# Performance work log

Hardware: AMD Instinct MI355X
Metric: run time of the kernel (lower is better)

## Reference

```python
import jax, jax.numpy as jnp
import numpy as np

B, T, D = 4096, 8, 2048
EPS = 1e-5


def setup_inputs() -> dict:
    key = jax.random.key(0)
    ks = jax.random.split(key, 7)
    s = 1.0 / np.sqrt(D)  # xavier-ish scale
    return {
        "H": jax.random.normal(ks[0], (B, T, D), jnp.float32),
        "Wq": jax.random.normal(ks[1], (T, D, D), jnp.float32) * s,
        "Wk": jax.random.normal(ks[2], (D, D), jnp.float32) * s,
        "Wv": jax.random.normal(ks[3], (D, D), jnp.float32) * s,
        "Wg": jax.random.normal(ks[4], (T, D, D), jnp.float32) * s,
        "bg": jnp.zeros((T, D), jnp.float32),
        "gamma": jnp.ones((T, D), jnp.float32),
        "beta": jnp.zeros((T, D), jnp.float32),
    }


def reference(H, Wq, Wk, Wv, Wg, bg, gamma, beta):
    # H: (B, T, D) = stacked task_reprs. Linear uses y = x @ W.T.
    scale = jnp.sqrt(jnp.asarray(D, H.dtype))
    K = jnp.einsum('bsd,ed->bse', H, Wk)          # (B, T, D) shared keys
    V = jnp.einsum('bsd,ed->bse', H, Wv)          # (B, T, D) shared values
    Q = jnp.einsum('btd,ted->bte', H, Wq)         # per-task query projection
    scores = jnp.einsum('bte,bse->bts', Q, K) / scale  # (B, T, T)
    attn = jax.nn.softmax(scores, axis=-1)
    ctx = jnp.einsum('bts,bse->bte', attn, V)     # (B, T, D)
    # dropout is identity at eval time
    g = jax.nn.sigmoid(jnp.einsum('btd,ted->bte', H, Wg) + bg)  # per-task gate
    x = H + g * ctx                               # gated residual
    mu = jnp.mean(x, axis=-1, keepdims=True)
    var = jnp.var(x, axis=-1, keepdims=True)
    out = (x - mu) / jnp.sqrt(var + EPS) * gamma + beta  # per-task LayerNorm
    return out
```

## Files before the change

kernel.cpp:

```cpp
#include <hip/hip_runtime.h>
#include <cstdint>

typedef unsigned short u16;
typedef uint32_t u32;
typedef float f32x4 __attribute__((ext_vector_type(4)));
typedef __bf16 bf16x8 __attribute__((ext_vector_type(8)));

#define GLDS16(gp, lp)                                                                   \
  __builtin_amdgcn_global_load_lds((const __attribute__((address_space(1))) void*)(gp),  \
                                   (__attribute__((address_space(3))) void*)(lp), 16, 0, 0)

__device__ __forceinline__ float blo(u32 u) { return __uint_as_float(u << 16); }
__device__ __forceinline__ float bhi(u32 u) { return __uint_as_float(u & 0xFFFF0000u); }
__device__ __forceinline__ u16 f2b(float f) {
  u32 u = __float_as_uint(f);
  u32 r = u + 0x7FFFu + ((u >> 16) & 1u);
  return (u16)(r >> 16);
}

__global__ __launch_bounds__(256) void ctil_cvt_f2b(
    const float* __restrict__ in, u16* __restrict__ out, long n)
{
  long i = ((long)blockIdx.x * blockDim.x + threadIdx.x) * 8;
  const long stride = (long)gridDim.x * blockDim.x * 8;
  for (; i < n; i += stride) {
    float4 a = *reinterpret_cast<const float4*>(in + i);
    float4 b = *reinterpret_cast<const float4*>(in + i + 4);
    uint4 o;
    o.x = (u32)f2b(a.x) | ((u32)f2b(a.y) << 16);
    o.y = (u32)f2b(a.z) | ((u32)f2b(a.w) << 16);
    o.z = (u32)f2b(b.x) | ((u32)f2b(b.y) << 16);
    o.w = (u32)f2b(b.z) | ((u32)f2b(b.w) << 16);
    *reinterpret_cast<uint4*>(out + i) = o;
  }
}

__global__ __launch_bounds__(256) void ctil_gemm_bt(
    const u16* __restrict__ Hb, const u16* __restrict__ Wqb,
    const u16* __restrict__ Wkb, const u16* __restrict__ Wvb,
    const u16* __restrict__ Wgb,
    u16* __restrict__ Kb, u16* __restrict__ Vb,
    u16* __restrict__ Qb, u16* __restrict__ Gb,
    int zbase)
{
  const int z = blockIdx.z + zbase;
  const u16* A;
  const u16* W;
  u16* C;
  int lda, ldc;
  if (z < 2) {
    A = Hb; lda = 2048; ldc = 2048;
    W = (z == 0) ? Wkb : Wvb;
    C = (z == 0) ? Kb : Vb;
  } else {
    const int t = (z - 2) & 7;
    A = Hb + t * 2048; lda = 16384; ldc = 16384;
    W = ((z < 10) ? Wqb : Wgb) + (size_t)t * (size_t)(2048 * 2048);
    C = ((z < 10) ? Qb : Gb) + t * 2048;
  }
  const int bm = blockIdx.x, bn = blockIdx.y;
  const int tid = (int)threadIdx.x;
  const int lane = tid & 63, wid = tid >> 6;
  const int wm = wid >> 1, wn = wid & 1;

  __shared__ __align__(16) u16 As[128 * 32];
  __shared__ __align__(16) u16 Bs[128 * 32];

  const int srow = tid >> 2;
  const int scol = (tid & 3) * 8;
  const u16* Ag = A + (size_t)(bm * 128 + srow) * lda + scol;
  const u16* Bg = W + (size_t)(bn * 128 + srow) * 2048 + scol;
  u16* AsW = As + wid * 512;
  u16* BsW = Bs + wid * 512;

  f32x4 acc[4][4] = {};

  const int frow = lane & 15;
  const int fk = (lane >> 4) * 8;

  for (int kt = 0; kt < 2048; kt += 32) {
    GLDS16(Ag + kt, AsW);
    GLDS16(Ag + kt + (size_t)64 * lda, AsW + 2048);
    GLDS16(Bg + kt, BsW);
    GLDS16(Bg + kt + 64 * 2048, BsW + 2048);
    __syncthreads();

    bf16x8 af[4], bfr[4];
#pragma unroll
    for (int i = 0; i < 4; ++i)
      af[i] = *reinterpret_cast<const bf16x8*>(&As[(wm * 64 + i * 16 + frow) * 32 + fk]);
#pragma unroll
    for (int j = 0; j < 4; ++j)
      bfr[j] = *reinterpret_cast<const bf16x8*>(&Bs[(wn * 64 + j * 16 + frow) * 32 + fk]);
#pragma unroll
    for (int i = 0; i < 4; ++i)
#pragma unroll
      for (int j = 0; j < 4; ++j)
        acc[i][j] = __builtin_amdgcn_mfma_f32_16x16x32_bf16(af[i], bfr[j], acc[i][j], 0, 0, 0);
    __syncthreads();
  }

  const int cl = lane & 15, chq = lane >> 4;
#pragma unroll
  for (int i = 0; i < 4; ++i) {
#pragma unroll
    for (int r = 0; r < 4; ++r) {
      const int row = bm * 128 + wm * 64 + i * 16 + chq * 4 + r;
      u16* Cr = C + (size_t)row * ldc + bn * 128 + wn * 64 + cl;
#pragma unroll
      for (int j = 0; j < 4; ++j)
        Cr[j * 16] = f2b(acc[i][j][r]);
    }
  }
}

__global__ __launch_bounds__(256) void ctil_epilogue(
    const u16* __restrict__ Hb, const u16* __restrict__ Kb,
    const u16* __restrict__ Vb, const u16* __restrict__ Qb,
    const u16* __restrict__ Gb, const float* __restrict__ bgp,
    const float* __restrict__ gap, const float* __restrict__ bep,
    float* __restrict__ Out)
{
  const int b = blockIdx.x;
  const int tid = (int)threadIdx.x;
  const int lane = tid & 63, wid = tid >> 6;
  const size_t rbase = (size_t)b * 16384;
  const int e0 = tid * 8;

  __shared__ float red[256];
  __shared__ float r1s[4], r2s[4];

  u32 qw[8][4], kw[8][4];
#pragma unroll
  for (int t = 0; t < 8; ++t) {
    uint4 v = *reinterpret_cast<const uint4*>(Qb + rbase + t * 2048 + e0);
    qw[t][0] = v.x; qw[t][1] = v.y; qw[t][2] = v.z; qw[t][3] = v.w;
    uint4 w = *reinterpret_cast<const uint4*>(Kb + rbase + t * 2048 + e0);
    kw[t][0] = w.x; kw[t][1] = w.y; kw[t][2] = w.z; kw[t][3] = w.w;
  }

  float sc[64];
#pragma unroll
  for (int p = 0; p < 64; ++p) sc[p] = 0.f;

#pragma unroll
  for (int c = 0; c < 4; ++c) {
    float ql[8], qh[8], kl[8], kh[8];
#pragma unroll
    for (int t = 0; t < 8; ++t) {
      ql[t] = blo(qw[t][c]); qh[t] = bhi(qw[t][c]);
      kl[t] = blo(kw[t][c]); kh[t] = bhi(kw[t][c]);
    }
#pragma unroll
    for (int t = 0; t < 8; ++t)
#pragma unroll
      for (int s = 0; s < 8; ++s)
        sc[t * 8 + s] += ql[t] * kl[s] + qh[t] * kh[s];
  }

#pragma unroll
  for (int p = 0; p < 64; ++p) {
    float v = sc[p];
#pragma unroll
    for (int m = 1; m < 64; m <<= 1) v += __shfl_xor(v, m, 64);
    sc[p] = v;
  }
  if (lane == 0) {
#pragma unroll
    for (int p = 0; p < 64; ++p) red[wid * 64 + p] = sc[p];
  }
  __syncthreads();

  const float INVS = 0.022097086912079608f;
#pragma unroll
  for (int p = 0; p < 64; ++p)
    sc[p] = (red[p] + red[64 + p] + red[128 + p] + red[192 + p]) * INVS;

#pragma unroll
  for (int t = 0; t < 8; ++t) {
    float m = sc[t * 8];
#pragma unroll
    for (int s = 1; s < 8; ++s) m = fmaxf(m, sc[t * 8 + s]);
    float l = 0.f;
#pragma unroll
    for (int s = 0; s < 8; ++s) {
      float e = __expf(sc[t * 8 + s] - m);
      sc[t * 8 + s] = e;
      l += e;
    }
    float inv = 1.f / l;
#pragma unroll
    for (int s = 0; s < 8; ++s) sc[t * 8 + s] *= inv;
  }

  u32 vw[8][4];
#pragma unroll
  for (int s = 0; s < 8; ++s) {
    uint4 v = *reinterpret_cast<const uint4*>(Vb + rbase + s * 2048 + e0);
    vw[s][0] = v.x; vw[s][1] = v.y; vw[s][2] = v.z; vw[s][3] = v.w;
  }

  for (int t = 0; t < 8; ++t) {
    float cx[8];
#pragma unroll
    for (int j = 0; j < 8; ++j) cx[j] = 0.f;
#pragma unroll
    for (int s = 0; s < 8; ++s) {
      float a = sc[t * 8 + s];
#pragma unroll
      for (int c = 0; c < 4; ++c) {
        cx[2 * c]     += a * blo(vw[s][c]);
        cx[2 * c + 1] += a * bhi(vw[s][c]);
      }
    }
    uint4 gu = *reinterpret_cast<const uint4*>(Gb + rbase + t * 2048 + e0);
    uint4 hu = *reinterpret_cast<const uint4*>(Hb + rbase + t * 2048 + e0);
    u32 ga[4] = {gu.x, gu.y, gu.z, gu.w};
    u32 ha[4] = {hu.x, hu.y, hu.z, hu.w};
    float bgv[8];
    *reinterpret_cast<float4*>(&bgv[0]) = *reinterpret_cast<const float4*>(bgp + t * 2048 + e0);
    *reinterpret_cast<float4*>(&bgv[4]) = *reinterpret_cast<const float4*>(bgp + t * 2048 + e0 + 4);
    float x[8];
    float s1 = 0.f, s2 = 0.f;
#pragma unroll
    for (int c = 0; c < 4; ++c) {
      float gl = blo(ga[c]) + bgv[2 * c];
      float gh = bhi(ga[c]) + bgv[2 * c + 1];
      float sgl = 1.f / (1.f + __expf(-gl));
      float sgh = 1.f / (1.f + __expf(-gh));
      float xl = blo(ha[c]) + sgl * cx[2 * c];
      float xh = bhi(ha[c]) + sgh * cx[2 * c + 1];
      x[2 * c] = xl; x[2 * c + 1] = xh;
      s1 += xl + xh;
      s2 += xl * xl + xh * xh;
    }
#pragma unroll
    for (int m = 1; m < 64; m <<= 1) {
      s1 += __shfl_xor(s1, m, 64);
      s2 += __shfl_xor(s2, m, 64);
    }
    if (lane == 0) { r1s[wid] = s1; r2s[wid] = s2; }
    __syncthreads();
    const float invD = 1.f / 2048.f;
    float S1 = r1s[0] + r1s[1] + r1s[2] + r1s[3];
    float S2 = r2s[0] + r2s[1] + r2s[2] + r2s[3];
    float mu = S1 * invD;
    float var = S2 * invD - mu * mu;
    float rstd = rsqrtf(var + 1e-5f);
    float gmv[8], btv[8];
    *reinterpret_cast<float4*>(&gmv[0]) = *reinterpret_cast<const float4*>(gap + t * 2048 + e0);
    *reinterpret_cast<float4*>(&gmv[4]) = *reinterpret_cast<const float4*>(gap + t * 2048 + e0 + 4);
    *reinterpret_cast<float4*>(&btv[0]) = *reinterpret_cast<const float4*>(bep + t * 2048 + e0);
    *reinterpret_cast<float4*>(&btv[4]) = *reinterpret_cast<const float4*>(bep + t * 2048 + e0 + 4);
    float4 o1, o2;
    o1.x = (x[0] - mu) * rstd * gmv[0] + btv[0];
    o1.y = (x[1] - mu) * rstd * gmv[1] + btv[1];
    o1.z = (x[2] - mu) * rstd * gmv[2] + btv[2];
    o1.w = (x[3] - mu) * rstd * gmv[3] + btv[3];
    o2.x = (x[4] - mu) * rstd * gmv[4] + btv[4];
    o2.y = (x[5] - mu) * rstd * gmv[5] + btv[5];
    o2.z = (x[6] - mu) * rstd * gmv[6] + btv[6];
    o2.w = (x[7] - mu) * rstd * gmv[7] + btv[7];
    *reinterpret_cast<float4*>(Out + rbase + t * 2048 + e0) = o1;
    *reinterpret_cast<float4*>(Out + rbase + t * 2048 + e0 + 4) = o2;
    __syncthreads();
  }
}

extern "C" void kernel_launch(void* const* d_in, const int* in_sizes, int n_in,
                              void* d_out, int out_size, void* d_ws, size_t ws_size,
                              hipStream_t stream)
{
  const float* H  = (const float*)d_in[0];
  const float* Wq = (const float*)d_in[1];
  const float* Wk = (const float*)d_in[2];
  const float* Wv = (const float*)d_in[3];
  const float* Wg = (const float*)d_in[4];
  const float* bg = (const float*)d_in[5];
  const float* ga = (const float*)d_in[6];
  const float* be = (const float*)d_in[7];
  float* Out = (float*)d_out;

  const size_t NWQ = 33554432, NWK = 4194304;
  u16* Wqb = (u16*)d_ws;
  u16* Wgb = Wqb + NWQ;
  u16* Wkb = Wgb + NWQ;
  u16* Wvb = Wkb + NWK;
  u16* chunkbase = Wvb + NWK;

  const size_t fixed = 150994944ull;
  int nch = 1;
  while (nch < 32 && fixed + (size_t)(4096 / nch) * 163840ull > ws_size) nch <<= 1;
  const int CB = 4096 / nch;

  u16* Hb = chunkbase;
  u16* Kw = Hb + (size_t)CB * 16384;
  u16* Vw = Kw + (size_t)CB * 16384;
  u16* Gw = Vw + (size_t)CB * 16384;
  u16* Qw = Gw + (size_t)CB * 16384;

  ctil_cvt_f2b<<<2048, 256, 0, stream>>>(Wq, Wqb, (long)NWQ);
  ctil_cvt_f2b<<<2048, 256, 0, stream>>>(Wg, Wgb, (long)NWQ);
  ctil_cvt_f2b<<<512, 256, 0, stream>>>(Wk, Wkb, (long)NWK);
  ctil_cvt_f2b<<<512, 256, 0, stream>>>(Wv, Wvb, (long)NWK);

  for (int c = 0; c < nch; ++c) {
    const size_t off = (size_t)c * (size_t)CB * 16384;
    ctil_cvt_f2b<<<2048, 256, 0, stream>>>(H + off, Hb, (long)CB * 16384);
    ctil_gemm_bt<<<dim3(CB / 16, 16, 2), 256, 0, stream>>>(
        Hb, Wqb, Wkb, Wvb, Wgb, Kw, Vw, Qw, Gw, 0);
    ctil_gemm_bt<<<dim3(CB / 128, 16, 16), 256, 0, stream>>>(
        Hb, Wqb, Wkb, Wvb, Wgb, Kw, Vw, Qw, Gw, 2);
    ctil_epilogue<<<dim3(CB), 256, 0, stream>>>(
        Hb, Kw, Vw, Qw, Gw, bg, ga, be, Out + off);
  }
}
```

Measured before the change: 1.839 ms.

## Replace bf16 GEMM with double-buffered 256x256-tile, 8-wave pipelined MFMA kernel

Replaces the 128x128, single-buffered GEMM with a 256x256-tile kernel using 512 threads and a 64-wide K step. Shared-memory stages are double-buffered with an XOR swizzle against bank conflicts. Global-to-LDS loads for the next K step are interleaved with four MFMA quadrants under explicit waitcnt, barriers and s_setprio. The goal is more data reuse per byte loaded and latency hiding that the old two-barrier loop lacked. The cost is 128KB of LDS per block, which limits occupancy, and the chunk count is capped at 16 so the tile divides the chunk.

```diff
diff --git a/kernel.cpp b/kernel.cpp
--- a/kernel.cpp
+++ b/kernel.cpp
@@ -35,7 +35,7 @@
   }
 }
 
-__global__ __launch_bounds__(256) void ctil_gemm_bt(
+__global__ __launch_bounds__(512, 2) void ctil_gemm256(
     const u16* __restrict__ Hb, const u16* __restrict__ Wqb,
     const u16* __restrict__ Wkb, const u16* __restrict__ Wvb,
     const u16* __restrict__ Wgb,
@@ -61,57 +61,147 @@
   const int bm = blockIdx.x, bn = blockIdx.y;
   const int tid = (int)threadIdx.x;
   const int lane = tid & 63, wid = tid >> 6;
-  const int wm = wid >> 1, wn = wid & 1;
-
-  __shared__ __align__(16) u16 As[128 * 32];
-  __shared__ __align__(16) u16 Bs[128 * 32];
-
-  const int srow = tid >> 2;
-  const int scol = (tid & 3) * 8;
-  const u16* Ag = A + (size_t)(bm * 128 + srow) * lda + scol;
-  const u16* Bg = W + (size_t)(bn * 128 + srow) * 2048 + scol;
-  u16* AsW = As + wid * 512;
-  u16* BsW = Bs + wid * 512;
-
-  f32x4 acc[4][4] = {};
-
-  const int frow = lane & 15;
-  const int fk = (lane >> 4) * 8;
-
-  for (int kt = 0; kt < 2048; kt += 32) {
-    GLDS16(Ag + kt, AsW);
-    GLDS16(Ag + kt + (size_t)64 * lda, AsW + 2048);
-    GLDS16(Bg + kt, BsW);
-    GLDS16(Bg + kt + 64 * 2048, BsW + 2048);
-    __syncthreads();
-
-    bf16x8 af[4], bfr[4];
-#pragma unroll
-    for (int i = 0; i < 4; ++i)
-      af[i] = *reinterpret_cast<const bf16x8*>(&As[(wm * 64 + i * 16 + frow) * 32 + fk]);
-#pragma unroll
-    for (int j = 0; j < 4; ++j)
-      bfr[j] = *reinterpret_cast<const bf16x8*>(&Bs[(wn * 64 + j * 16 + frow) * 32 + fk]);
-#pragma unroll
-    for (int i = 0; i < 4; ++i)
-#pragma unroll
-      for (int j = 0; j < 4; ++j)
-        acc[i][j] = __builtin_amdgcn_mfma_f32_16x16x32_bf16(af[i], bfr[j], acc[i][j], 0, 0, 0);
-    __syncthreads();
-  }
-
-  const int cl = lane & 15, chq = lane >> 4;
-#pragma unroll
-  for (int i = 0; i < 4; ++i) {
+  const int wm = wid >> 2, wn = wid & 3;
+
+  __shared__ __align__(16) u16 As[2][16384];
+  __shared__ __align__(16) u16 Bs[2][16384];
+
+  const int srl = lane >> 3;
+  const int sq  = (lane & 7) ^ srl;
+  const u16* Ag = A + (size_t)(bm * 256 + wid * 8 + srl) * lda + sq * 8;
+  const u16* Bg = W + (size_t)(bn * 256 + wid * 8 + srl) * 2048 + sq * 8;
+
+#define STAGE(buf, kt, h)                                                     \
+  do {                                                                        \
+    GLDS16(Ag + (size_t)((h) * 64) * lda + (kt) * 64,                         \
+           &As[buf][((h) * 64 + wid * 8) * 64]);                              \
+    GLDS16(Bg + (size_t)((h) * 64) * 2048 + (kt) * 64,                        \
+           &Bs[buf][((h) * 64 + wid * 8) * 64]);                              \
+  } while (0)
+
+  const int la = lane & 15, g = lane >> 4, x = lane & 7;
+  const int arow = wm * 128 + la;
+  const int brow = wn * 64 + la;
+  const int sl0 = (g ^ x) << 3;
+  const int sl1 = ((4 | g) ^ x) << 3;
+
+  bf16x8 aR[4][2];
+  bf16x8 bR[2][2][2];
+  f32x4 acc[8][4] = {};
+
+#define DSA(buf, mh)                                                          \
+  do {                                                                        \
+    _Pragma("unroll") for (int j = 0; j < 4; ++j) {                           \
+      const int r_ = (arow + (mh) * 64 + j * 16) * 64;                        \
+      aR[j][0] = *reinterpret_cast<const bf16x8*>(&As[buf][r_ + sl0]);        \
+      aR[j][1] = *reinterpret_cast<const bf16x8*>(&As[buf][r_ + sl1]);        \
+    }                                                                         \
+  } while (0)
+
+#define DSB(buf, nh)                                                          \
+  do {                                                                        \
+    _Pragma("unroll") for (int j = 0; j < 2; ++j) {                           \
+      const int r_ = (brow + (nh) * 32 + j * 16) * 64;                        \
+      bR[nh][j][0] = *reinterpret_cast<const bf16x8*>(&Bs[buf][r_ + sl0]);    \
+      bR[nh][j][1] = *reinterpret_cast<const bf16x8*>(&Bs[buf][r_ + sl1]);    \
+    }                                                                         \
+  } while (0)
+
+#define MFMA16(mh, nh)                                                        \
+  do {                                                                        \
+    _Pragma("unroll") for (int j = 0; j < 4; ++j)                             \
+    _Pragma("unroll") for (int jj = 0; jj < 2; ++jj)                          \
+    _Pragma("unroll") for (int ks = 0; ks < 2; ++ks)                          \
+      acc[(mh) * 4 + j][(nh) * 2 + jj] =                                      \
+          __builtin_amdgcn_mfma_f32_16x16x32_bf16(                            \
+              aR[j][ks], bR[nh][jj][ks], acc[(mh) * 4 + j][(nh) * 2 + jj],    \
+              0, 0, 0);                                                       \
+  } while (0)
+
+#define BAR()                                                                 \
+  do {                                                                        \
+    __builtin_amdgcn_s_barrier();                                             \
+    asm volatile("" ::: "memory");                                            \
+  } while (0)
+#define LGKM0()                                                               \
+  do {                                                                        \
+    asm volatile("s_waitcnt lgkmcnt(0)" ::: "memory");                        \
+    __builtin_amdgcn_sched_barrier(0);                                        \
+  } while (0)
+
+#pragma unroll
+  for (int h = 0; h < 4; ++h) STAGE(0, 0, h);
+
+#pragma unroll 1
+  for (int it = 0; it < 16; ++it) {
+    const int k1 = 2 * it + 1, k2 = 2 * it + 2;
+    const bool nl = (it < 15);
+    STAGE(1, k1, 0);
+    asm volatile("s_waitcnt vmcnt(2)" ::: "memory");
+    BAR();
+    DSA(0, 0); DSB(0, 0);
+    LGKM0();
+    __builtin_amdgcn_s_setprio(1); MFMA16(0, 0); __builtin_amdgcn_s_setprio(0);
+    BAR();
+    DSB(0, 1);
+    STAGE(1, k1, 1);
+    BAR(); LGKM0();
+    __builtin_amdgcn_s_setprio(1); MFMA16(0, 1); __builtin_amdgcn_s_setprio(0);
+    BAR();
+    DSA(0, 1);
+    STAGE(1, k1, 2);
+    BAR(); LGKM0();
+    __builtin_amdgcn_s_setprio(1); MFMA16(1, 1); __builtin_amdgcn_s_setprio(0);
+    BAR();
+    STAGE(1, k1, 3);
+    BAR(); LGKM0();
+    __builtin_amdgcn_s_setprio(1); MFMA16(1, 0); __builtin_amdgcn_s_setprio(0);
+    BAR();
+    if (nl) {
+      STAGE(0, k2, 0);
+      asm volatile("s_waitcnt vmcnt(2)" ::: "memory");
+    } else {
+      asm volatile("s_waitcnt vmcnt(0)" ::: "memory");
+    }
+    BAR();
+    DSA(1, 0); DSB(1, 0);
+    LGKM0();
+    __builtin_amdgcn_s_setprio(1); MFMA16(0, 0); __builtin_amdgcn_s_setprio(0);
+    BAR();
+    DSB(1, 1);
+    if (nl) STAGE(0, k2, 1);
+    BAR(); LGKM0();
+    __builtin_amdgcn_s_setprio(1); MFMA16(0, 1); __builtin_amdgcn_s_setprio(0);
+    BAR();
+    DSA(1, 1);
+    if (nl) STAGE(0, k2, 2);
+    BAR(); LGKM0();
+    __builtin_amdgcn_s_setprio(1); MFMA16(1, 1); __builtin_amdgcn_s_setprio(0);
+    BAR();
+    if (nl) STAGE(0, k2, 3);
+    BAR(); LGKM0();
+    __builtin_amdgcn_s_setprio(1); MFMA16(1, 0); __builtin_amdgcn_s_setprio(0);
+    BAR();
+  }
+
+  const int cl = lane & 15, cq = lane >> 4;
+#pragma unroll
+  for (int mf = 0; mf < 8; ++mf) {
 #pragma unroll
     for (int r = 0; r < 4; ++r) {
-      const int row = bm * 128 + wm * 64 + i * 16 + chq * 4 + r;
-      u16* Cr = C + (size_t)row * ldc + bn * 128 + wn * 64 + cl;
-#pragma unroll
-      for (int j = 0; j < 4; ++j)
-        Cr[j * 16] = f2b(acc[i][j][r]);
-    }
-  }
+      const int row = bm * 256 + wm * 128 + mf * 16 + cq * 4 + r;
+      u16* Cr = C + (size_t)row * ldc + bn * 256 + wn * 64 + cl;
+#pragma unroll
+      for (int nf = 0; nf < 4; ++nf)
+        Cr[nf * 16] = f2b(acc[mf][nf][r]);
+    }
+  }
+#undef STAGE
+#undef DSA
+#undef DSB
+#undef MFMA16
+#undef BAR
+#undef LGKM0
 }
 
 __global__ __launch_bounds__(256) void ctil_epilogue(
@@ -290,7 +380,7 @@
 
   const size_t fixed = 150994944ull;
   int nch = 1;
-  while (nch < 32 && fixed + (size_t)(4096 / nch) * 163840ull > ws_size) nch <<= 1;
+  while (nch < 16 && fixed + (size_t)(4096 / nch) * 163840ull > ws_size) nch <<= 1;
   const int CB = 4096 / nch;
 
   u16* Hb = chunkbase;
@@ -307,9 +397,9 @@
   for (int c = 0; c < nch; ++c) {
     const size_t off = (size_t)c * (size_t)CB * 16384;
     ctil_cvt_f2b<<<2048, 256, 0, stream>>>(H + off, Hb, (long)CB * 16384);
-    ctil_gemm_bt<<<dim3(CB / 16, 16, 2), 256, 0, stream>>>(
+    ctil_gemm256<<<dim3(CB / 32, 8, 2), 512, 0, stream>>>(
         Hb, Wqb, Wkb, Wvb, Wgb, Kw, Vw, Qw, Gw, 0);
-    ctil_gemm_bt<<<dim3(CB / 128, 16, 16), 256, 0, stream>>>(
+    ctil_gemm256<<<dim3(CB / 256, 8, 16), 512, 0, stream>>>(
         Hb, Wqb, Wkb, Wvb, Wgb, Kw, Vw, Qw, Gw, 2);
     ctil_epilogue<<<dim3(CB), 256, 0, stream>>>(
         Hb, Kw, Vw, Qw, Gw, bg, ga, be, Out + off);
```

After: 1.717 ms. 1.07x faster.
